# Performance work log

Measured on AMD Instinct MI355X. Metric: run time of the kernel, lower is better.

## Reference

```python
import jax, jax.numpy as jnp
import numpy as np

EMBED_DIM = 1024
NUM_HEADS = 16
HEAD_DIM = EMBED_DIM // NUM_HEADS


def setup_inputs() -> dict:
    key = jax.random.key(0)
    ks = jax.random.split(key, 9)
    s = 1.0 / np.sqrt(EMBED_DIM)
    x = jax.random.normal(ks[0], (2, 2048, EMBED_DIM), dtype=jnp.float32)
    Wq = jax.random.uniform(ks[1], (EMBED_DIM, EMBED_DIM), jnp.float32, -s, s)
    bq = jax.random.uniform(ks[2], (EMBED_DIM,), jnp.float32, -s, s)
    Wk = jax.random.uniform(ks[3], (EMBED_DIM, EMBED_DIM), jnp.float32, -s, s)
    bk = jax.random.uniform(ks[4], (EMBED_DIM,), jnp.float32, -s, s)
    Wv = jax.random.uniform(ks[5], (EMBED_DIM, EMBED_DIM), jnp.float32, -s, s)
    bv = jax.random.uniform(ks[6], (EMBED_DIM,), jnp.float32, -s, s)
    Wo = jax.random.uniform(ks[7], (EMBED_DIM, EMBED_DIM), jnp.float32, -s, s)
    bo = jax.random.uniform(ks[8], (EMBED_DIM,), jnp.float32, -s, s)
    return {"x": x, "Wq": Wq, "bq": bq, "Wk": Wk, "bk": bk,
            "Wv": Wv, "bv": bv, "Wo": Wo, "bo": bo}


def reference(x, Wq, bq, Wk, bk, Wv, bv, Wo, bo):
    B, S, E = x.shape
    H, D = NUM_HEADS, HEAD_DIM
    # Linear projections (torch Linear: y = x @ W.T + b; here W stored as [in,out])
    Q = (x @ Wq + bq).reshape(B, S, H, D).transpose(0, 2, 1, 3)  # [B,H,S,D]
    K = (x @ Wk + bk).reshape(B, S, H, D).transpose(0, 2, 1, 3)
    V = (x @ Wv + bv).reshape(B, S, H, D).transpose(0, 2, 1, 3)
    scale = jnp.sqrt(jnp.asarray(D, dtype=jnp.float32))
    energy = jnp.einsum("bhqd,bhkd->bhqk", Q, K) / scale  # [B,H,S,S]
    attn = jax.nn.softmax(energy, axis=-1)
    out = jnp.einsum("bhqk,bhkd->bhqd", attn, V)  # [B,H,S,D]
    out = out.transpose(0, 2, 1, 3).reshape(B, S, E)
    return out @ Wo + bo
```

## Files before the change

### kernel.cpp

```cpp
#include <hip/hip_runtime.h>
#include <cstdint>
#include <cstddef>

#define S_LEN 2048
#define NHEAD 16
#define HDIM  64
#define EMB   1024
#define MROWS 4096
#define KDIM  1024

typedef __bf16 bf16;
typedef __attribute__((ext_vector_type(8))) __bf16 bf16x8;
typedef __attribute__((ext_vector_type(4))) __bf16 bf16x4;
typedef __attribute__((ext_vector_type(4))) float  f32x4;

__device__ __forceinline__ f32x4 mfma_16x16x32(bf16x8 a, bf16x8 b, f32x4 c) {
  return __builtin_amdgcn_mfma_f32_16x16x32_bf16(a, b, c, 0, 0, 0);
}

__device__ __forceinline__ void gload16(const bf16* g, void* lds_uniform) {
  __builtin_amdgcn_global_load_lds(
      (const __attribute__((address_space(1))) void*)g,
      (__attribute__((address_space(3))) void*)lds_uniform, 16, 0, 0);
}

__global__ void prep_x_kernel(const float* __restrict__ x, bf16* __restrict__ xb) {
  int idx = blockIdx.x * blockDim.x + threadIdx.x;
  const float4* x4 = (const float4*)x;
  float4 a = x4[idx * 2 + 0];
  float4 b = x4[idx * 2 + 1];
  bf16x8 v;
  v[0] = (bf16)a.x; v[1] = (bf16)a.y; v[2] = (bf16)a.z; v[3] = (bf16)a.w;
  v[4] = (bf16)b.x; v[5] = (bf16)b.y; v[6] = (bf16)b.z; v[7] = (bf16)b.w;
  *(bf16x8*)(xb + (size_t)idx * 8) = v;
}

__global__ void prep_w_kernel(const float* __restrict__ Wq, const float* __restrict__ Wk,
                              const float* __restrict__ Wv, const float* __restrict__ Wo,
                              bf16* __restrict__ wqkvt, bf16* __restrict__ wot) {
  __shared__ float tile[64][65];
  int mat = blockIdx.z;
  const float* W = (mat == 0) ? Wq : (mat == 1) ? Wk : (mat == 2) ? Wv : Wo;
  bf16* dst = (mat < 3) ? (wqkvt + (size_t)mat * 1024 * 1024) : wot;
  int k0 = blockIdx.x * 64, r0 = blockIdx.y * 64;
  int tid = threadIdx.x;
#pragma unroll
  for (int i = 0; i < 16; i++) {
    int idx = i * 256 + tid;
    int kk = idx >> 6, rr = idx & 63;
    tile[kk][rr] = W[(size_t)(k0 + kk) * 1024 + r0 + rr];
  }
  __syncthreads();
#pragma unroll
  for (int i = 0; i < 16; i++) {
    int idx = i * 256 + tid;
    int rr = idx >> 6, kk = idx & 63;
    dst[(size_t)(r0 + rr) * 1024 + k0 + kk] = (bf16)tile[kk][rr];
  }
}

template <int MODE>
__global__ __launch_bounds__(256, 2) void gemm_bt(
    const bf16* __restrict__ A, const bf16* __restrict__ Bt,
    const float* __restrict__ b0, const float* __restrict__ b1, const float* __restrict__ b2,
    float* __restrict__ outf,
    bf16* __restrict__ qo, bf16* __restrict__ ko, bf16* __restrict__ vto) {
  __shared__ bf16 lA[128 * 64];
  __shared__ bf16 lB[128 * 64];
  const int bm = blockIdx.x, bn = blockIdx.y;
  const int tid = threadIdx.x;
  const int w = tid >> 6, l = tid & 63;
  const int wm = w >> 1, wn = w & 1;
  const int lr = l & 15, lg = l >> 4;

  f32x4 zero = {0.f, 0.f, 0.f, 0.f};
  f32x4 acc[4][4];
#pragma unroll
  for (int i = 0; i < 4; i++)
#pragma unroll
    for (int j = 0; j < 4; j++) acc[i][j] = zero;

  char* lAb = (char*)lA;
  char* lBb = (char*)lB;
  const size_t a_row0 = (size_t)bm * 128;
  const size_t b_row0 = (size_t)bn * 128;

  for (int kt = 0; kt < KDIM; kt += 64) {
    __syncthreads();
#pragma unroll
    for (int i = 0; i < 4; i++) {
      int cq = i * 256 + tid;
      int row = cq >> 3;
      int c8 = (cq & 7) ^ (row & 7);
      gload16(A + (a_row0 + row) * KDIM + kt + c8 * 8, lAb + (i * 256 + w * 64) * 16);
    }
#pragma unroll
    for (int i = 0; i < 4; i++) {
      int cq = i * 256 + tid;
      int row = cq >> 3;
      int c8 = (cq & 7) ^ (row & 7);
      gload16(Bt + (b_row0 + row) * KDIM + kt + c8 * 8, lBb + (i * 256 + w * 64) * 16);
    }
    asm volatile("s_waitcnt vmcnt(0)" ::: "memory");
    __syncthreads();

#pragma unroll
    for (int kk = 0; kk < 2; kk++) {
      bf16x8 af[4], bfv[4];
#pragma unroll
      for (int i = 0; i < 4; i++) {
        int row = wm * 64 + i * 16 + lr;
        af[i] = *(const bf16x8*)(lAb + row * 128 + ((((kk << 2) + lg) ^ (row & 7)) << 4));
      }
#pragma unroll
      for (int j = 0; j < 4; j++) {
        int row = wn * 64 + j * 16 + lr;
        bfv[j] = *(const bf16x8*)(lBb + row * 128 + ((((kk << 2) + lg) ^ (row & 7)) << 4));
      }
#pragma unroll
      for (int i = 0; i < 4; i++)
#pragma unroll
        for (int j = 0; j < 4; j++) acc[i][j] = mfma_16x16x32(af[i], bfv[j], acc[i][j]);
    }
  }

#pragma unroll
  for (int i = 0; i < 4; i++) {
#pragma unroll
    for (int j = 0; j < 4; j++) {
      int n = bn * 128 + wn * 64 + j * 16 + lr;
      int mbase = bm * 128 + wm * 64 + i * 16 + lg * 4;
      if (MODE == 1) {
#pragma unroll
        for (int jj = 0; jj < 4; jj++)
          outf[(size_t)(mbase + jj) * 1024 + n] = acc[i][j][jj] + b0[n];
      } else {
        int p = n >> 10, nn = n & 1023;
        int h = nn >> 6, d = nn & 63;
        int b = mbase >> 11, s = mbase & 2047;
        const float* bp = (p == 0) ? b0 : (p == 1) ? b1 : b2;
        float bias = bp[nn];
        if (p == 2) {
          bf16x4 pk;
#pragma unroll
          for (int jj = 0; jj < 4; jj++) pk[jj] = (bf16)(acc[i][j][jj] + bias);
          *(bf16x4*)(vto + (((size_t)(b * 16 + h)) * 64 + d) * 2048 + s) = pk;
        } else {
          float qsc = (p == 0) ? 0.18033688011112042f : 1.0f;
          bf16* o = (p == 0) ? qo : ko;
#pragma unroll
          for (int jj = 0; jj < 4; jj++)
            o[(((size_t)(b * 16 + h)) * 2048 + s + jj) * 64 + d] =
                (bf16)((acc[i][j][jj] + bias) * qsc);
        }
      }
    }
  }
}

__global__ __launch_bounds__(256, 4) void attn_kernel(
    const bf16* __restrict__ qb, const bf16* __restrict__ kb,
    const bf16* __restrict__ vtb, bf16* __restrict__ ob) {
  __shared__ bf16 lK[2 * 64 * 64];
  __shared__ bf16 lV[2 * 64 * 64];
  __shared__ bf16 lP[4 * 16 * 64];
  const int qt = blockIdx.x;
  const int bh = blockIdx.y;
  const int tid = threadIdx.x;
  const int w = tid >> 6, l = tid & 63;
  const int lr = l & 15, lg = l >> 4;

  const bf16* Qh = qb + (size_t)bh * S_LEN * HDIM;
  const bf16* Kh = kb + (size_t)bh * S_LEN * HDIM;
  const bf16* Vh = vtb + (size_t)bh * HDIM * S_LEN;

  const int qrow = qt * 64 + w * 16 + lr;
  bf16x8 qf0 = *(const bf16x8*)(Qh + (size_t)qrow * 64 + lg * 8);
  bf16x8 qf1 = *(const bf16x8*)(Qh + (size_t)qrow * 64 + 32 + lg * 8);

  bf16x8 ones;
#pragma unroll
  for (int i = 0; i < 8; i++) ones[i] = (bf16)1.0f;

  f32x4 zero = {0.f, 0.f, 0.f, 0.f};
  f32x4 o_acc[4];
  f32x4 l_acc = zero;
#pragma unroll
  for (int t = 0; t < 4; t++) o_acc[t] = zero;

  char* lKb = (char*)lK;
  char* lVb = (char*)lV;

  const int rbase = lr * 128;
  const int cs0 = (lg ^ (lr & 7)) << 4;
  const int cs1 = ((4 + lg) ^ (lr & 7)) << 4;
  const int pwo = rbase + ((lg & 1) << 3) + (((lg >> 1) ^ (lr & 7)) << 4);
  char* pwbase = (char*)lP + w * 2048;

  const int row0 = tid >> 3;
  const int c8b = ((tid & 7) ^ (row0 & 7)) << 3;
  int koff = row0 * HDIM + c8b;
  int voff = row0 * S_LEN + c8b;
  char* lkd = lKb + w * 1024;
  char* lvd = lVb + w * 1024;

#define STAGE(B)                                                              \
  {                                                                           \
    gload16(Kh + koff,         lkd + (B));                                    \
    gload16(Kh + koff + 2048,  lkd + (B) + 4096);                             \
    gload16(Vh + voff,         lvd + (B));                                    \
    gload16(Vh + voff + 65536, lvd + (B) + 4096);                             \
    koff += 4096;                                                             \
    voff += 64;                                                               \
  }

#define QK(dst, off)                                                          \
  {                                                                           \
    bf16x8 k0_ = *(const bf16x8*)(kB + rbase + (off) + cs0);                  \
    bf16x8 k1_ = *(const bf16x8*)(kB + rbase + (off) + cs1);                  \
    f32x4 z_ = zero;                                                          \
    z_ = mfma_16x16x32(k0_, qf0, z_);                                         \
    dst = mfma_16x16x32(k1_, qf1, z_);                                        \
  }

#define PEXP(scv, n16)                                                        \
  {                                                                           \
    bf16x4 pk_;                                                               \
    pk_[0] = (bf16)__builtin_amdgcn_exp2f(scv[0]);                            \
    pk_[1] = (bf16)__builtin_amdgcn_exp2f(scv[1]);                            \
    pk_[2] = (bf16)__builtin_amdgcn_exp2f(scv[2]);                            \
    pk_[3] = (bf16)__builtin_amdgcn_exp2f(scv[3]);                            \
    *(bf16x4*)(pwbase + (pwo ^ ((n16) << 5))) = pk_;                          \
  }

#define COMPUTE(B)                                                            \
  {                                                                           \
    const char* kB = lKb + (B);                                               \
    const char* vB = lVb + (B);                                               \
    f32x4 s0, s1, s2, s3;                                                     \
    __builtin_amdgcn_s_setprio(1);                                            \
    QK(s0, 0); QK(s1, 2048); QK(s2, 4096); QK(s3, 6144);                      \
    __builtin_amdgcn_s_setprio(0);                                            \
    PEXP(s0, 0); PEXP(s1, 1); PEXP(s2, 2); PEXP(s3, 3);                       \
    bf16x8 pf0 = *(const bf16x8*)(pwbase + rbase + cs0);                      \
    bf16x8 pf1 = *(const bf16x8*)(pwbase + rbase + cs1);                      \
    __builtin_amdgcn_s_setprio(1);                                            \
    l_acc = mfma_16x16x32(pf0, ones, l_acc);                                  \
    l_acc = mfma_16x16x32(pf1, ones, l_acc);                                  \
    {                                                                         \
      bf16x8 vf0 = *(const bf16x8*)(vB + rbase + 0 + cs0);                    \
      bf16x8 vf1 = *(const bf16x8*)(vB + rbase + 0 + cs1);                    \
      o_acc[0] = mfma_16x16x32(pf0, vf0, o_acc[0]);                           \
      o_acc[0] = mfma_16x16x32(pf1, vf1, o_acc[0]);                           \
    }                                                                         \
    {                                                                         \
      bf16x8 vf0 = *(const bf16x8*)(vB + rbase + 2048 + cs0);                 \
      bf16x8 vf1 = *(const bf16x8*)(vB + rbase + 2048 + cs1);                 \
      o_acc[1] = mfma_16x16x32(pf0, vf0, o_acc[1]);                           \
      o_acc[1] = mfma_16x16x32(pf1, vf1, o_acc[1]);                           \
    }                                                                         \
    {                                                                         \
      bf16x8 vf0 = *(const bf16x8*)(vB + rbase + 4096 + cs0);                 \
      bf16x8 vf1 = *(const bf16x8*)(vB + rbase + 4096 + cs1);                 \
      o_acc[2] = mfma_16x16x32(pf0, vf0, o_acc[2]);                           \
      o_acc[2] = mfma_16x16x32(pf1, vf1, o_acc[2]);                           \
    }                                                                         \
    {                                                                         \
      bf16x8 vf0 = *(const bf16x8*)(vB + rbase + 6144 + cs0);                 \
      bf16x8 vf1 = *(const bf16x8*)(vB + rbase + 6144 + cs1);                 \
      o_acc[3] = mfma_16x16x32(pf0, vf0, o_acc[3]);                           \
      o_acc[3] = mfma_16x16x32(pf1, vf1, o_acc[3]);                           \
    }                                                                         \
    __builtin_amdgcn_s_setprio(0);                                            \
  }

#define SYNC                                                                  \
  asm volatile("s_waitcnt vmcnt(0)" ::: "memory");                            \
  __syncthreads();

  STAGE(0);
  SYNC;

  for (int t = 0; t < 30; t += 2) {
    STAGE(8192);
    COMPUTE(0);
    SYNC;
    STAGE(0);
    COMPUTE(8192);
    SYNC;
  }
  STAGE(8192);
  COMPUTE(0);
  SYNC;
  COMPUTE(8192);

#undef STAGE
#undef QK
#undef PEXP
#undef COMPUTE
#undef SYNC

  const int b = bh >> 4, h = bh & 15;
  float r0 = 1.0f / l_acc[0];
  float r1 = 1.0f / l_acc[1];
  float r2 = 1.0f / l_acc[2];
  float r3 = 1.0f / l_acc[3];
#pragma unroll
  for (int n16 = 0; n16 < 4; n16++) {
    int s = qt * 64 + w * 16 + lg * 4;
    int d = n16 * 16 + lr;
    size_t base = ((size_t)(b * 2048 + s)) * 1024 + h * 64 + d;
    ob[base]        = (bf16)(o_acc[n16][0] * r0);
    ob[base + 1024] = (bf16)(o_acc[n16][1] * r1);
    ob[base + 2048] = (bf16)(o_acc[n16][2] * r2);
    ob[base + 3072] = (bf16)(o_acc[n16][3] * r3);
  }
}

extern "C" void kernel_launch(void* const* d_in, const int* in_sizes, int n_in,
                              void* d_out, int out_size, void* d_ws, size_t ws_size,
                              hipStream_t stream) {
  const float* x  = (const float*)d_in[0];
  const float* Wq = (const float*)d_in[1];
  const float* bq = (const float*)d_in[2];
  const float* Wk = (const float*)d_in[3];
  const float* bk = (const float*)d_in[4];
  const float* Wv = (const float*)d_in[5];
  const float* bv = (const float*)d_in[6];
  const float* Wo = (const float*)d_in[7];
  const float* bo = (const float*)d_in[8];
  float* out = (float*)d_out;

  char* ws = (char*)d_ws;
  bf16* xb    = (bf16*)(ws + (size_t)(0)  * (1 << 20));
  bf16* wqkvt = (bf16*)(ws + (size_t)(8)  * (1 << 20));
  bf16* wot   = (bf16*)(ws + (size_t)(14) * (1 << 20));
  bf16* qbuf  = (bf16*)(ws + (size_t)(16) * (1 << 20));
  bf16* kbuf  = (bf16*)(ws + (size_t)(24) * (1 << 20));
  bf16* vtbuf = (bf16*)(ws + (size_t)(32) * (1 << 20));
  bf16* obuf  = (bf16*)(ws + (size_t)(40) * (1 << 20));

  prep_x_kernel<<<dim3(2048), dim3(256), 0, stream>>>(x, xb);
  prep_w_kernel<<<dim3(16, 16, 4), dim3(256), 0, stream>>>(Wq, Wk, Wv, Wo, wqkvt, wot);
  gemm_bt<0><<<dim3(32, 24), dim3(256), 0, stream>>>(xb, wqkvt, bq, bk, bv,
                                                     nullptr, qbuf, kbuf, vtbuf);
  attn_kernel<<<dim3(32, 32), dim3(256), 0, stream>>>(qbuf, kbuf, vtbuf, obuf);
  gemm_bt<1><<<dim3(32, 8), dim3(256), 0, stream>>>(obuf, wot, bo, nullptr, nullptr,
                                                    out, nullptr, nullptr, nullptr);
}
```

Measured before the change: 107.1 us.

## Switch attention to 32x32x16 MFMA with register-resident P via permlane swap

Rewrites the attention inner loop to use 32x32x16 bf16 MFMA with two waves per block, each owning 32 query rows. The exponentiated score tile is packed with v_cvt_pk_bf16 and rearranged into the A-operand layout using v_permlane32_swap, so P no longer round-trips through LDS. Staging loads are doubled per thread because of the smaller block. The aim is fewer LDS accesses and MFMA instructions per tile, at the cost of more registers per wave and a smaller 128-thread block with launch bounds of 2.

```diff
diff --git a/kernel.cpp b/kernel.cpp
--- a/kernel.cpp
+++ b/kernel.cpp
@@ -10,12 +10,29 @@
 #define KDIM  1024
 
 typedef __bf16 bf16;
-typedef __attribute__((ext_vector_type(8))) __bf16 bf16x8;
-typedef __attribute__((ext_vector_type(4))) __bf16 bf16x4;
-typedef __attribute__((ext_vector_type(4))) float  f32x4;
+typedef unsigned int u32;
+typedef __attribute__((ext_vector_type(8)))  __bf16 bf16x8;
+typedef __attribute__((ext_vector_type(4)))  __bf16 bf16x4;
+typedef __attribute__((ext_vector_type(4)))  float  f32x4;
+typedef __attribute__((ext_vector_type(16))) float  f32x16;
+typedef __attribute__((ext_vector_type(4)))  u32    u32x4;
 
 __device__ __forceinline__ f32x4 mfma_16x16x32(bf16x8 a, bf16x8 b, f32x4 c) {
   return __builtin_amdgcn_mfma_f32_16x16x32_bf16(a, b, c, 0, 0, 0);
+}
+__device__ __forceinline__ f32x16 mfma32(bf16x8 a, bf16x8 b, f32x16 c) {
+  return __builtin_amdgcn_mfma_f32_32x32x16_bf16(a, b, c, 0, 0, 0);
+}
+__device__ __forceinline__ u32 cvt_pk_bf16(float lo, float hi) {
+  u32 r;
+  asm("v_cvt_pk_bf16_f32 %0, %1, %2" : "=v"(r) : "v"(lo), "v"(hi));
+  return r;
+}
+__device__ __forceinline__ f32x16 fz16() {
+  f32x16 z;
+#pragma unroll
+  for (int i = 0; i < 16; i++) z[i] = 0.f;
+  return z;
 }
 
 __device__ __forceinline__ void gload16(const bf16* g, void* lds_uniform) {
@@ -158,44 +175,42 @@
   }
 }
 
-__global__ __launch_bounds__(256, 4) void attn_kernel(
+__global__ __launch_bounds__(128, 2) void attn_kernel(
     const bf16* __restrict__ qb, const bf16* __restrict__ kb,
     const bf16* __restrict__ vtb, bf16* __restrict__ ob) {
   __shared__ bf16 lK[2 * 64 * 64];
   __shared__ bf16 lV[2 * 64 * 64];
-  __shared__ bf16 lP[4 * 16 * 64];
   const int qt = blockIdx.x;
   const int bh = blockIdx.y;
   const int tid = threadIdx.x;
   const int w = tid >> 6, l = tid & 63;
-  const int lr = l & 15, lg = l >> 4;
+  const int l5 = l >> 5, l31 = l & 31;
 
   const bf16* Qh = qb + (size_t)bh * S_LEN * HDIM;
   const bf16* Kh = kb + (size_t)bh * S_LEN * HDIM;
   const bf16* Vh = vtb + (size_t)bh * HDIM * S_LEN;
 
-  const int qrow = qt * 64 + w * 16 + lr;
-  bf16x8 qf0 = *(const bf16x8*)(Qh + (size_t)qrow * 64 + lg * 8);
-  bf16x8 qf1 = *(const bf16x8*)(Qh + (size_t)qrow * 64 + 32 + lg * 8);
+  const int qrow = qt * 64 + w * 32 + l31;
+  const bf16* qp = Qh + (size_t)qrow * 64 + l5 * 8;
+  bf16x8 qf0 = *(const bf16x8*)(qp);
+  bf16x8 qf1 = *(const bf16x8*)(qp + 16);
+  bf16x8 qf2 = *(const bf16x8*)(qp + 32);
+  bf16x8 qf3 = *(const bf16x8*)(qp + 48);
 
   bf16x8 ones;
 #pragma unroll
   for (int i = 0; i < 8; i++) ones[i] = (bf16)1.0f;
 
-  f32x4 zero = {0.f, 0.f, 0.f, 0.f};
-  f32x4 o_acc[4];
-  f32x4 l_acc = zero;
-#pragma unroll
-  for (int t = 0; t < 4; t++) o_acc[t] = zero;
+  f32x16 o0 = fz16(), o1 = fz16(), lsum = fz16();
 
   char* lKb = (char*)lK;
   char* lVb = (char*)lV;
 
-  const int rbase = lr * 128;
-  const int cs0 = (lg ^ (lr & 7)) << 4;
-  const int cs1 = ((4 + lg) ^ (lr & 7)) << 4;
-  const int pwo = rbase + ((lg & 1) << 3) + (((lg >> 1) ^ (lr & 7)) << 4);
-  char* pwbase = (char*)lP + w * 2048;
+  const int rb = l31 * 128;
+  const int cso0 = (((0 + l5) ^ (l & 7)) << 4);
+  const int cso1 = (((2 + l5) ^ (l & 7)) << 4);
+  const int cso2 = (((4 + l5) ^ (l & 7)) << 4);
+  const int cso3 = (((6 + l5) ^ (l & 7)) << 4);
 
   const int row0 = tid >> 3;
   const int c8b = ((tid & 7) ^ (row0 & 7)) << 3;
@@ -207,69 +222,85 @@
 #define STAGE(B)                                                              \
   {                                                                           \
     gload16(Kh + koff,         lkd + (B));                                    \
+    gload16(Kh + koff + 1024,  lkd + (B) + 2048);                             \
     gload16(Kh + koff + 2048,  lkd + (B) + 4096);                             \
+    gload16(Kh + koff + 3072,  lkd + (B) + 6144);                             \
     gload16(Vh + voff,         lvd + (B));                                    \
+    gload16(Vh + voff + 32768, lvd + (B) + 2048);                             \
     gload16(Vh + voff + 65536, lvd + (B) + 4096);                             \
+    gload16(Vh + voff + 98304, lvd + (B) + 6144);                             \
     koff += 4096;                                                             \
     voff += 64;                                                               \
   }
 
-#define QK(dst, off)                                                          \
+#define QKHALF(B, H, paA, paB)                                                \
   {                                                                           \
-    bf16x8 k0_ = *(const bf16x8*)(kB + rbase + (off) + cs0);                  \
-    bf16x8 k1_ = *(const bf16x8*)(kB + rbase + (off) + cs1);                  \
-    f32x4 z_ = zero;                                                          \
-    z_ = mfma_16x16x32(k0_, qf0, z_);                                         \
-    dst = mfma_16x16x32(k1_, qf1, z_);                                        \
-  }
-
-#define PEXP(scv, n16)                                                        \
-  {                                                                           \
-    bf16x4 pk_;                                                               \
-    pk_[0] = (bf16)__builtin_amdgcn_exp2f(scv[0]);                            \
-    pk_[1] = (bf16)__builtin_amdgcn_exp2f(scv[1]);                            \
-    pk_[2] = (bf16)__builtin_amdgcn_exp2f(scv[2]);                            \
-    pk_[3] = (bf16)__builtin_amdgcn_exp2f(scv[3]);                            \
-    *(bf16x4*)(pwbase + (pwo ^ ((n16) << 5))) = pk_;                          \
+    const char* kB_ = lKb + (B) + (H) * 4096;                                 \
+    f32x16 s = fz16();                                                        \
+    __builtin_amdgcn_s_setprio(1);                                            \
+    bf16x8 kf0 = *(const bf16x8*)(kB_ + rb + cso0);                           \
+    bf16x8 kf1 = *(const bf16x8*)(kB_ + rb + cso1);                           \
+    bf16x8 kf2 = *(const bf16x8*)(kB_ + rb + cso2);                           \
+    bf16x8 kf3 = *(const bf16x8*)(kB_ + rb + cso3);                           \
+    s = mfma32(kf0, qf0, s);                                                  \
+    s = mfma32(kf1, qf1, s);                                                  \
+    s = mfma32(kf2, qf2, s);                                                  \
+    s = mfma32(kf3, qf3, s);                                                  \
+    __builtin_amdgcn_s_setprio(0);                                            \
+    _Pragma("unroll") for (int r = 0; r < 16; r++)                            \
+      s[r] = __builtin_amdgcn_exp2f(s[r]);                                    \
+    {                                                                         \
+      u32 a_ = cvt_pk_bf16(s[0], s[1]);                                       \
+      u32 b_ = cvt_pk_bf16(s[2], s[3]);                                       \
+      u32 c_ = cvt_pk_bf16(s[4], s[5]);                                       \
+      u32 d_ = cvt_pk_bf16(s[6], s[7]);                                       \
+      asm("v_permlane32_swap_b32 %0, %1" : "+v"(a_), "+v"(c_));               \
+      asm("v_permlane32_swap_b32 %0, %1" : "+v"(b_), "+v"(d_));               \
+      u32x4 t_ = {a_, b_, c_, d_};                                            \
+      paA = __builtin_bit_cast(bf16x8, t_);                                   \
+    }                                                                         \
+    {                                                                         \
+      u32 a_ = cvt_pk_bf16(s[8], s[9]);                                       \
+      u32 b_ = cvt_pk_bf16(s[10], s[11]);                                     \
+      u32 c_ = cvt_pk_bf16(s[12], s[13]);                                     \
+      u32 d_ = cvt_pk_bf16(s[14], s[15]);                                     \
+      asm("v_permlane32_swap_b32 %0, %1" : "+v"(a_), "+v"(c_));               \
+      asm("v_permlane32_swap_b32 %0, %1" : "+v"(b_), "+v"(d_));               \
+      u32x4 t_ = {a_, b_, c_, d_};                                            \
+      paB = __builtin_bit_cast(bf16x8, t_);                                   \
+    }                                                                         \
   }
 
 #define COMPUTE(B)                                                            \
   {                                                                           \
-    const char* kB = lKb + (B);                                               \
-    const char* vB = lVb + (B);                                               \
-    f32x4 s0, s1, s2, s3;                                                     \
+    bf16x8 pa0, pa1, pa2, pa3;                                                \
+    QKHALF(B, 0, pa0, pa1);                                                   \
+    QKHALF(B, 1, pa2, pa3);                                                   \
+    const char* vB_ = lVb + (B);                                              \
     __builtin_amdgcn_s_setprio(1);                                            \
-    QK(s0, 0); QK(s1, 2048); QK(s2, 4096); QK(s3, 6144);                      \
-    __builtin_amdgcn_s_setprio(0);                                            \
-    PEXP(s0, 0); PEXP(s1, 1); PEXP(s2, 2); PEXP(s3, 3);                       \
-    bf16x8 pf0 = *(const bf16x8*)(pwbase + rbase + cs0);                      \
-    bf16x8 pf1 = *(const bf16x8*)(pwbase + rbase + cs1);                      \
-    __builtin_amdgcn_s_setprio(1);                                            \
-    l_acc = mfma_16x16x32(pf0, ones, l_acc);                                  \
-    l_acc = mfma_16x16x32(pf1, ones, l_acc);                                  \
+    lsum = mfma32(pa0, ones, lsum);                                           \
+    lsum = mfma32(pa1, ones, lsum);                                           \
+    lsum = mfma32(pa2, ones, lsum);                                           \
+    lsum = mfma32(pa3, ones, lsum);                                           \
     {                                                                         \
-      bf16x8 vf0 = *(const bf16x8*)(vB + rbase + 0 + cs0);                    \
-      bf16x8 vf1 = *(const bf16x8*)(vB + rbase + 0 + cs1);                    \
-      o_acc[0] = mfma_16x16x32(pf0, vf0, o_acc[0]);                           \
-      o_acc[0] = mfma_16x16x32(pf1, vf1, o_acc[0]);                           \
+      bf16x8 vf0 = *(const bf16x8*)(vB_ + rb + cso0);                         \
+      bf16x8 vf1 = *(const bf16x8*)(vB_ + rb + cso1);                         \
+      bf16x8 vf2 = *(const bf16x8*)(vB_ + rb + cso2);                         \
+      bf16x8 vf3 = *(const bf16x8*)(vB_ + rb + cso3);                         \
+      o0 = mfma32(pa0, vf0, o0);                                              \
+      o0 = mfma32(pa1, vf1, o0);                                              \
+      o0 = mfma32(pa2, vf2, o0);                                              \
+      o0 = mfma32(pa3, vf3, o0);                                              \
     }                                                                         \
     {                                                                         \
-      bf16x8 vf0 = *(const bf16x8*)(vB + rbase + 2048 + cs0);                 \
-      bf16x8 vf1 = *(const bf16x8*)(vB + rbase + 2048 + cs1);                 \
-      o_acc[1] = mfma_16x16x32(pf0, vf0, o_acc[1]);                           \
-      o_acc[1] = mfma_16x16x32(pf1, vf1, o_acc[1]);                           \
-    }                                                                         \
-    {                                                                         \
-      bf16x8 vf0 = *(const bf16x8*)(vB + rbase + 4096 + cs0);                 \
-      bf16x8 vf1 = *(const bf16x8*)(vB + rbase + 4096 + cs1);                 \
-      o_acc[2] = mfma_16x16x32(pf0, vf0, o_acc[2]);                           \
-      o_acc[2] = mfma_16x16x32(pf1, vf1, o_acc[2]);                           \
-    }                                                                         \
-    {                                                                         \
-      bf16x8 vf0 = *(const bf16x8*)(vB + rbase + 6144 + cs0);                 \
-      bf16x8 vf1 = *(const bf16x8*)(vB + rbase + 6144 + cs1);                 \
-      o_acc[3] = mfma_16x16x32(pf0, vf0, o_acc[3]);                           \
-      o_acc[3] = mfma_16x16x32(pf1, vf1, o_acc[3]);                           \
+      bf16x8 vf0 = *(const bf16x8*)(vB_ + 4096 + rb + cso0);                  \
+      bf16x8 vf1 = *(const bf16x8*)(vB_ + 4096 + rb + cso1);                  \
+      bf16x8 vf2 = *(const bf16x8*)(vB_ + 4096 + rb + cso2);                  \
+      bf16x8 vf3 = *(const bf16x8*)(vB_ + 4096 + rb + cso3);                  \
+      o1 = mfma32(pa0, vf0, o1);                                              \
+      o1 = mfma32(pa1, vf1, o1);                                              \
+      o1 = mfma32(pa2, vf2, o1);                                              \
+      o1 = mfma32(pa3, vf3, o1);                                              \
     }                                                                         \
     __builtin_amdgcn_s_setprio(0);                                            \
   }
@@ -295,25 +326,19 @@
   COMPUTE(8192);
 
 #undef STAGE
-#undef QK
-#undef PEXP
+#undef QKHALF
 #undef COMPUTE
 #undef SYNC
 
   const int b = bh >> 4, h = bh & 15;
-  float r0 = 1.0f / l_acc[0];
-  float r1 = 1.0f / l_acc[1];
-  float r2 = 1.0f / l_acc[2];
-  float r3 = 1.0f / l_acc[3];
-#pragma unroll
-  for (int n16 = 0; n16 < 4; n16++) {
-    int s = qt * 64 + w * 16 + lg * 4;
-    int d = n16 * 16 + lr;
-    size_t base = ((size_t)(b * 2048 + s)) * 1024 + h * 64 + d;
-    ob[base]        = (bf16)(o_acc[n16][0] * r0);
-    ob[base + 1024] = (bf16)(o_acc[n16][1] * r1);
-    ob[base + 2048] = (bf16)(o_acc[n16][2] * r2);
-    ob[base + 3072] = (bf16)(o_acc[n16][3] * r3);
+#pragma unroll
+  for (int r = 0; r < 16; r++) {
+    int q = (r & 3) + 8 * (r >> 2) + 4 * l5;
+    int s = qt * 64 + w * 32 + q;
+    float inv = 1.0f / lsum[r];
+    size_t base = ((size_t)(b * 2048 + s)) * 1024 + h * 64 + l31;
+    ob[base]      = (bf16)(o0[r] * inv);
+    ob[base + 32] = (bf16)(o1[r] * inv);
   }
 }
 
@@ -344,7 +369,7 @@
   prep_w_kernel<<<dim3(16, 16, 4), dim3(256), 0, stream>>>(Wq, Wk, Wv, Wo, wqkvt, wot);
   gemm_bt<0><<<dim3(32, 24), dim3(256), 0, stream>>>(xb, wqkvt, bq, bk, bv,
                                                      nullptr, qbuf, kbuf, vtbuf);
-  attn_kernel<<<dim3(32, 32), dim3(256), 0, stream>>>(qbuf, kbuf, vtbuf, obuf);
+  attn_kernel<<<dim3(32, 32), dim3(128), 0, stream>>>(qbuf, kbuf, vtbuf, obuf);
   gemm_bt<1><<<dim3(32, 8), dim3(256), 0, stream>>>(obuf, wot, bo, nullptr, nullptr,
                                                     out, nullptr, nullptr, nullptr);
 }
```

After: 106.7 us. No clear change (-0.4%).
